# Kernel tuning notes

Hardware: AMD Instinct MI355X
Metric: run time of the kernel (lower is better)

Reference implementation:

```python
import jax, jax.numpy as jnp
import numpy as np

N = 50000
E = 1600000
HID = 128
H = 8
D = HID // H


def _layer_norm(x, g, b, eps=1e-5):
    mu = jnp.mean(x, axis=-1, keepdims=True)
    var = jnp.mean(jnp.square(x - mu), axis=-1, keepdims=True)
    return (x - mu) * jax.lax.rsqrt(var + eps) * g + b


def setup_inputs() -> dict:
    key = jax.random.key(0)
    ks = jax.random.split(key, 20)
    s = 1.0 / np.sqrt(HID)
    inp = {
        "x": jax.random.normal(ks[0], (N, HID), jnp.float32),
        "edge_index": jax.random.randint(ks[1], (2, E), 0, N, jnp.int64),
        "edge_attr": jax.random.randint(ks[2], (E,), 0, 13, jnp.int64),
        # projections (stored as [in, out] so y = x @ W + b)
        "Wq": jax.random.normal(ks[3], (HID, HID), jnp.float32) * s,
        "bq": jnp.zeros((HID,), jnp.float32),
        "Wk": jax.random.normal(ks[4], (HID, HID), jnp.float32) * s,
        "bk": jnp.zeros((HID,), jnp.float32),
        "Wv": jax.random.normal(ks[5], (HID, HID), jnp.float32) * s,
        "bv": jnp.zeros((HID,), jnp.float32),
        "Wo": jax.random.normal(ks[6], (HID, HID), jnp.float32) * s,
        "bo": jnp.zeros((HID,), jnp.float32),
        "edge_bias_table": jax.random.normal(ks[7], (13, H), jnp.float32) * 0.02,
        "W1": jax.random.normal(ks[8], (HID, 4 * HID), jnp.float32) * s,
        "b1": jnp.zeros((4 * HID,), jnp.float32),
        "W2": jax.random.normal(ks[9], (4 * HID, HID), jnp.float32) * (0.5 * s),
        "b2": jnp.zeros((HID,), jnp.float32),
        "g1": jnp.ones((HID,), jnp.float32),
        "be1": jnp.zeros((HID,), jnp.float32),
        "g2": jnp.ones((HID,), jnp.float32),
        "be2": jnp.zeros((HID,), jnp.float32),
    }
    return inp


def reference(x, edge_index, edge_attr, Wq, bq, Wk, bk, Wv, bv, Wo, bo,
              edge_bias_table, W1, b1, W2, b2, g1, be1, g2, be2):
    n = x.shape[0]
    residual = x
    h = _layer_norm(x, g1, be1)
    Q = (h @ Wq + bq).reshape(n, H, D)
    K = (h @ Wk + bk).reshape(n, H, D)
    V = (h @ Wv + bv).reshape(n, H, D)
    src, dst = edge_index[0], edge_index[1]
    # per-edge scores [E, H]
    scores = jnp.sum(Q[dst] * K[src], axis=-1) / np.sqrt(D)
    scores = scores + edge_bias_table[jnp.clip(edge_attr, 0, 12)]
    # scatter softmax over incoming edges of each dst (global max, as in source)
    scores_exp = jnp.exp(scores - jnp.max(scores))
    attn_sum = jax.ops.segment_sum(scores_exp, dst, num_segments=n)  # [N, H]
    attn_w = scores_exp / (attn_sum[dst] + 1e-8)                      # [E, H]
    messages = V[src] * attn_w[..., None]                             # [E, H, D]
    out = jax.ops.segment_sum(messages, dst, num_segments=n)          # [N, H, D]
    out = out.reshape(n, HID) @ Wo + bo
    x = residual + out  # dropout is identity in eval
    residual = x
    h2 = _layer_norm(x, g2, be2)
    ffn = jax.nn.relu(h2 @ W1 + b1) @ W2 + b2
    return residual + ffn
```

## Files before the change

### kernel.cpp

```cpp
#include <hip/hip_runtime.h>
#include <hip/hip_bf16.h>

#define N_NODES 50000
#define E_EDGES 1600000
#define HID 128
#define NH 8
#define HD 16

#define NBKT 196
#define BKT_CAP 9216
#define CHUNK_A 4096
#define EPT 16

using short8 = __attribute__((ext_vector_type(8))) short;
using f32x4  = __attribute__((ext_vector_type(4))) float;
using f32x2  = __attribute__((ext_vector_type(2))) float;
typedef _Float16 h16x2 __attribute__((ext_vector_type(2)));

#if defined(__has_builtin) && __has_builtin(__builtin_amdgcn_fdot2)
#define FDOT2(a, b, c) __builtin_amdgcn_fdot2((a), (b), (c), false)
#else
__device__ __forceinline__ float FDOT2(h16x2 a, h16x2 b, float c) {
    return fmaf((float)a[0], (float)b[0], fmaf((float)a[1], (float)b[1], c));
}
#endif

__device__ __forceinline__ float wave_reduce_sum(float v) {
    #pragma unroll
    for (int off = 32; off > 0; off >>= 1) v += __shfl_xor(v, off, 64);
    return v;
}

__device__ __forceinline__ unsigned int packbf2(float a, float b) {
    __hip_bfloat162 t;
    t.x = __float2bfloat16(a);
    t.y = __float2bfloat16(b);
    unsigned int u;
    __builtin_memcpy(&u, &t, 4);
    return u;
}

__device__ __forceinline__ unsigned char fp8e(float v) {
    return (unsigned char)(__builtin_amdgcn_cvt_pk_fp8_f32(v, v, 0u, false) & 0xFFu);
}

__device__ __forceinline__ void cvt16(uint4 u, float* f) {
    f32x2 t;
    t = __builtin_amdgcn_cvt_pk_f32_fp8(u.x, false); f[0] = t[0];  f[1] = t[1];
    t = __builtin_amdgcn_cvt_pk_f32_fp8(u.x, true);  f[2] = t[0];  f[3] = t[1];
    t = __builtin_amdgcn_cvt_pk_f32_fp8(u.y, false); f[4] = t[0];  f[5] = t[1];
    t = __builtin_amdgcn_cvt_pk_f32_fp8(u.y, true);  f[6] = t[0];  f[7] = t[1];
    t = __builtin_amdgcn_cvt_pk_f32_fp8(u.z, false); f[8] = t[0];  f[9] = t[1];
    t = __builtin_amdgcn_cvt_pk_f32_fp8(u.z, true);  f[10] = t[0]; f[11] = t[1];
    t = __builtin_amdgcn_cvt_pk_f32_fp8(u.w, false); f[12] = t[0]; f[13] = t[1];
    t = __builtin_amdgcn_cvt_pk_f32_fp8(u.w, true);  f[14] = t[0]; f[15] = t[1];
}

union U4H {
    uint4 u;
    h16x2 h[4];
};

__global__ __launch_bounds__(256) void ln_kernel(const float* __restrict__ x,
                                                 const float* __restrict__ g,
                                                 const float* __restrict__ b,
                                                 __hip_bfloat16* __restrict__ out, int n) {
    int wave = threadIdx.x >> 6;
    int lane = threadIdx.x & 63;
    int row = blockIdx.x * 4 + wave;
    if (row >= n) return;
    float2 v = ((const float2*)(x + (size_t)row * HID))[lane];
    float s = wave_reduce_sum(v.x + v.y);
    float mu = s * (1.0f / HID);
    float dx = v.x - mu, dy = v.y - mu;
    float q = wave_reduce_sum(dx * dx + dy * dy);
    float rstd = rsqrtf(q * (1.0f / HID) + 1e-5f);
    float2 gg = ((const float2*)g)[lane];
    float2 bb = ((const float2*)b)[lane];
    __hip_bfloat162 o;
    o.x = __float2bfloat16(dx * rstd * gg.x + bb.x);
    o.y = __float2bfloat16(dy * rstd * gg.y + bb.y);
    ((__hip_bfloat162*)(out + (size_t)row * HID))[lane] = o;
}

__global__ __launch_bounds__(256) void wcvt_all(const float* __restrict__ Wq,
                                                const float* __restrict__ Wk,
                                                const float* __restrict__ Wv,
                                                const float* __restrict__ Wo,
                                                const float* __restrict__ W1,
                                                const float* __restrict__ W2,
                                                const float* __restrict__ bq,
                                                const float* __restrict__ bk,
                                                const float* __restrict__ bv,
                                                __hip_bfloat16* __restrict__ Wqkvt,
                                                __hip_bfloat16* __restrict__ Wot,
                                                __hip_bfloat16* __restrict__ W1t,
                                                __hip_bfloat16* __restrict__ W2t,
                                                float* __restrict__ bqkv,
                                                int* __restrict__ bcur) {
    int t = blockIdx.x * 256 + threadIdx.x;
    if (t >= 196608) {
        int i = t - 196608;
        if (i < 384) bqkv[i] = i < 128 ? bq[i] : (i < 256 ? bk[i - 128] : bv[i - 256]);
        else if (i < 384 + NBKT) bcur[i - 384] = 0;
        return;
    }
    const float* W; __hip_bfloat16* Wt; int K, N, idx;
    if (t < 65536) {
        int which = t >> 14; idx = t & 16383; K = 128; N = 128;
        W = which == 0 ? Wq : which == 1 ? Wk : which == 2 ? Wv : Wo;
        Wt = which == 3 ? Wot : Wqkvt + which * 16384;
    } else if (t < 131072) { idx = t - 65536;  K = 128; N = 512; W = W1; Wt = W1t; }
    else                   { idx = t - 131072; K = 512; N = 128; W = W2; Wt = W2t; }
    int n = idx / K, k = idx - n * K;
    Wt[idx] = __float2bfloat16(W[(size_t)k * N + n]);
}

template <int K, int OB>
__global__ __launch_bounds__(512) void gemm_mfma(const __hip_bfloat16* __restrict__ A,
                                                 const __hip_bfloat16* __restrict__ Wt,
                                                 const float* __restrict__ bias,
                                                 const float* __restrict__ res,
                                                 float* __restrict__ C,
                                                 __hip_bfloat16* __restrict__ Cb,
                                                 _Float16* __restrict__ Chh,
                                                 unsigned char* __restrict__ C8,
                                                 const float* __restrict__ gw,
                                                 const float* __restrict__ bw,
                                                 int M, int NC, int relu) {
    __shared__ short8 smem[2048 + 2048];
    const int row0 = blockIdx.x * 128;
    const int col0 = blockIdx.y * 128;
    const int tid = threadIdx.x;
    const int w = tid >> 6, l = tid & 63;
    const int lr = l & 15, hi = l >> 4;
    f32x4 acc[8] = {};
    for (int kk = 0; kk < K / 128; ++kk) {
        #pragma unroll
        for (int it = 0; it < 4; ++it) {
            unsigned d = tid + it * 512;
            int r = d >> 4, sd = d & 15;
            int ss = sd ^ (r & 7);
            int gr = row0 + r; if (gr >= M) gr = M - 1;
            __builtin_amdgcn_global_load_lds(
                (const __attribute__((address_space(1))) void*)(A + (size_t)gr * K + kk * 128 + ss * 8),
                (__attribute__((address_space(3))) void*)(smem + (d & ~63u)),
                16, 0, 0);
        }
        #pragma unroll
        for (int it = 0; it < 4; ++it) {
            unsigned d = tid + it * 512;
            int r = d >> 4, sd = d & 15;
            int ss = sd ^ (r & 7);
            __builtin_amdgcn_global_load_lds(
                (const __attribute__((address_space(1))) void*)(Wt + (size_t)(col0 + r) * K + kk * 128 + ss * 8),
                (__attribute__((address_space(3))) void*)(smem + 2048 + (d & ~63u)),
                16, 0, 0);
        }
        __syncthreads();
        const int ar = w * 16 + lr;
        #pragma unroll
        for (int ks = 0; ks < 4; ++ks) {
            int s = ks * 4 + hi;
            short8 a = smem[ar * 16 + (s ^ (ar & 7))];
            #pragma unroll
            for (int f = 0; f < 8; ++f) {
                int br = f * 16 + lr;
                short8 b = smem[2048 + br * 16 + (s ^ (br & 7))];
                acc[f] = __builtin_amdgcn_mfma_f32_16x16x32_bf16(a, b, acc[f], 0, 0, 0);
            }
        }
        __syncthreads();
    }
    if (OB == 3) {
        float vv[8][4];
        float gc[8], bc[8];
        #pragma unroll
        for (int f = 0; f < 8; ++f) {
            int c = f * 16 + lr;
            gc[f] = gw[c]; bc[f] = bw[c];
            float bv = bias[c];
            #pragma unroll
            for (int j = 0; j < 4; ++j) {
                int r = row0 + w * 16 + hi * 4 + j;
                int rr = r < M ? r : M - 1;
                vv[f][j] = acc[f][j] + bv + res[(size_t)rr * NC + c];
            }
        }
        #pragma unroll
        for (int j = 0; j < 4; ++j) {
            int r = row0 + w * 16 + hi * 4 + j;
            float s = 0.f, qq = 0.f;
            #pragma unroll
            for (int f = 0; f < 8; ++f) { s += vv[f][j]; qq += vv[f][j] * vv[f][j]; }
            #pragma unroll
            for (int m = 1; m <= 8; m <<= 1) { s += __shfl_xor(s, m); qq += __shfl_xor(qq, m); }
            float mu = s * (1.0f / 128.0f);
            float rstd = rsqrtf(qq * (1.0f / 128.0f) - mu * mu + 1e-5f);
            if (r < M) {
                #pragma unroll
                for (int f = 0; f < 8; ++f) {
                    int c = f * 16 + lr;
                    C[(size_t)r * NC + c] = vv[f][j];
                    Cb[(size_t)r * NC + c] = __float2bfloat16((vv[f][j] - mu) * rstd * gc[f] + bc[f]);
                }
            }
        }
        return;
    }
    const float scl = (OB == 2 && blockIdx.y == 0) ? 0.25f : 1.0f;
    #pragma unroll
    for (int f = 0; f < 8; ++f) {
        int c = col0 + f * 16 + lr;
        float bv = bias[c];
        #pragma unroll
        for (int j = 0; j < 4; ++j) {
            int r = row0 + w * 16 + hi * 4 + j;
            if (r < M) {
                float v = acc[f][j] + bv;
                if (relu) v = fmaxf(v, 0.f);
                if (res) v += res[(size_t)r * NC + c];
                if (OB == 0) C[(size_t)r * NC + c] = v;
                else if (OB == 1) Cb[(size_t)r * NC + c] = __float2bfloat16(v);
                else {
                    if (blockIdx.y < 2)
                        Chh[(size_t)blockIdx.y * N_NODES * 128 + (size_t)r * 128 + (c & 127)] =
                            (_Float16)(v * scl);
                    else
                        C8[(size_t)r * 128 + (c & 127)] = fp8e(v);
                }
            }
        }
    }
}

__global__ __launch_bounds__(256) void binA_kernel(const int* __restrict__ ei,
                                                   const int* __restrict__ attr,
                                                   int* __restrict__ bcur,
                                                   unsigned int* __restrict__ temp) {
    __shared__ unsigned int sval[CHUNK_A];
    __shared__ unsigned short sbkt[CHUNK_A];
    __shared__ int hist[NBKT];
    __shared__ int lofs[NBKT];
    __shared__ int gbase[NBKT];
    __shared__ int lcur[NBKT];
    __shared__ int sc[256];
    const int tid = threadIdx.x;
    const int e0 = blockIdx.x * CHUNK_A;
    const int n = min(CHUNK_A, E_EDGES - e0);
    for (int i = tid; i < NBKT; i += 256) hist[i] = 0;
    __syncthreads();
    unsigned int v[EPT];
    short bk[EPT];
    #pragma unroll
    for (int j = 0; j < EPT; ++j) {
        int i = tid + j * 256;
        bk[j] = -1;
        v[j] = 0;
        if (i < n) {
            int e = e0 + i;
            int src = ei[e];
            int dst = ei[E_EDGES + e];
            int a = attr[e]; a = min(max(a, 0), 12);
            v[j] = (unsigned)src | ((unsigned)a << 16) | ((unsigned)(dst & 255) << 20);
            int b = dst >> 8;
            bk[j] = (short)b;
            atomicAdd(&hist[b], 1);
        }
    }
    __syncthreads();
    sc[tid] = (tid < NBKT) ? hist[tid] : 0;
    __syncthreads();
    for (int off = 1; off < 256; off <<= 1) {
        int x = (tid >= off) ? sc[tid - off] : 0;
        __syncthreads();
        sc[tid] += x;
        __syncthreads();
    }
    if (tid < NBKT) {
        int h = hist[tid];
        lofs[tid] = sc[tid] - h;
        lcur[tid] = 0;
        gbase[tid] = h ? atomicAdd(&bcur[tid], h) : 0;
    }
    __syncthreads();
    #pragma unroll
    for (int j = 0; j < EPT; ++j) {
        if (bk[j] >= 0) {
            int p = lofs[bk[j]] + atomicAdd(&lcur[bk[j]], 1);
            sval[p] = v[j];
            sbkt[p] = (unsigned short)bk[j];
        }
    }
    __syncthreads();
    for (int i = tid; i < n; i += 256) {
        int b = sbkt[i];
        temp[(size_t)b * BKT_CAP + gbase[b] + (i - lofs[b])] = sval[i];
    }
}

__global__ __launch_bounds__(1024) void binB_kernel(const int* __restrict__ bcur,
                                                    const unsigned int* __restrict__ temp,
                                                    unsigned int* __restrict__ packed,
                                                    int* __restrict__ offs) {
    __shared__ int cnts[256];
    __shared__ int hist[256];
    __shared__ int cur[256];
    const int b = blockIdx.x, tid = threadIdx.x;
    if (tid < 256) {
        cnts[tid] = (tid < NBKT) ? bcur[tid] : 0;
        hist[tid] = 0;
    }
    __syncthreads();
    for (int off = 1; off < 256; off <<= 1) {
        int x = 0;
        if (tid < 256 && tid >= off) x = cnts[tid - off];
        __syncthreads();
        if (tid < 256) cnts[tid] += x;
        __syncthreads();
    }
    const int cnt = bcur[b];
    const int start = cnts[b] - cnt;
    const size_t base = (size_t)b * BKT_CAP;
    for (int i = tid; i < cnt; i += 1024)
        atomicAdd(&hist[(temp[base + i] >> 20) & 255], 1);
    __syncthreads();
    if (tid < 256) cur[tid] = hist[tid];
    __syncthreads();
    for (int off = 1; off < 256; off <<= 1) {
        int x = 0;
        if (tid < 256 && tid >= off) x = cur[tid - off];
        __syncthreads();
        if (tid < 256) cur[tid] += x;
        __syncthreads();
    }
    const int node0 = b * 256;
    if (tid < 256) {
        int excl = cur[tid] - hist[tid];
        cur[tid] = excl;
        int node = node0 + tid;
        if (node < N_NODES) offs[node] = start + excl;
    }
    if (b == NBKT - 1 && tid == 0) offs[N_NODES] = start + cnt;
    __syncthreads();
    for (int i = tid; i < cnt; i += 1024) {
        unsigned int v = temp[base + i];
        int d = (v >> 20) & 255;
        int p = start + atomicAdd(&cur[d], 1);
        packed[p] = v & 0xFFFFFu;
    }
}

__global__ __launch_bounds__(256) void fused_attn_kernel(
    const unsigned int* __restrict__ packed,
    const int* __restrict__ offs,
    const _Float16* __restrict__ qkh,
    const unsigned char* __restrict__ v8p,
    const float* __restrict__ btab,
    __hip_bfloat16* __restrict__ out) {
    __shared__ float bLDS[104];
    const int tid = threadIdx.x;
    if (tid < 104) bLDS[tid] = btab[tid];
    __syncthreads();
    const int wave = tid >> 6, lane = tid & 63;
    const int n = blockIdx.x * 4 + wave;
    const int slot = lane >> 3, sub = lane & 7;
    const char* qh = (const char*)qkh;
    const char* kh = (const char*)(qkh + (size_t)N_NODES * 128);
    const unsigned sb = (unsigned)sub << 5;
    U4H q0, q1;
    q0.u = *(const uint4*)(qh + ((unsigned)n << 8) + sb);
    q1.u = *(const uint4*)(qh + ((unsigned)n << 8) + sb + 16u);
    const int lo = offs[n], hi = offs[n + 1];
    const int nit = (hi - lo + 7) >> 3;
    int i = lo + slot;
    float acc[16] = {};
    float wsum = 0.f;
    bool valid = i < hi;
    unsigned int pk = valid ? packed[i] : 0u;
    int i1 = i + 8;
    bool valid1 = i1 < hi;
    unsigned int pk1 = valid1 ? packed[i1] : 0u;
    unsigned src = pk & 0xFFFFu;
    U4H k0, k1;
    k0.u = *(const uint4*)(kh + (src << 8) + sb);
    k1.u = *(const uint4*)(kh + (src << 8) + sb + 16u);
    uint4 vc = *(const uint4*)(v8p + (src << 7) + (sb >> 1));
    for (int it = 0; it < nit; ++it) {
        const int i2 = i1 + 8;
        const bool valid2 = i2 < hi;
        const unsigned int pk2 = valid2 ? packed[i2] : 0u;
        const unsigned srcn = pk1 & 0xFFFFu;
        U4H kn0, kn1;
        kn0.u = *(const uint4*)(kh + (srcn << 8) + sb);
        kn1.u = *(const uint4*)(kh + (srcn << 8) + sb + 16u);
        uint4 vn = *(const uint4*)(v8p + (srcn << 7) + (sb >> 1));
        float p = 0.f;
        #pragma unroll
        for (int j = 0; j < 4; ++j) p = FDOT2(q0.h[j], k0.h[j], p);
        #pragma unroll
        for (int j = 0; j < 4; ++j) p = FDOT2(q1.h[j], k1.h[j], p);
        float s = p + bLDS[((pk >> 16) & 0xFu) * 8 + sub];
        float w = valid ? __expf(s) : 0.f;
        wsum += w;
        float v[16];
        cvt16(vc, v);
        #pragma unroll
        for (int j = 0; j < 16; ++j) acc[j] = fmaf(w, v[j], acc[j]);
        k0 = kn0; k1 = kn1; vc = vn;
        pk = pk1; valid = valid1;
        pk1 = pk2; valid1 = valid2; i1 = i2;
    }
    #pragma unroll
    for (int j = 0; j < 16; ++j) {
        acc[j] += __shfl_xor(acc[j], 8);
        acc[j] += __shfl_xor(acc[j], 16);
        acc[j] += __shfl_xor(acc[j], 32);
    }
    wsum += __shfl_xor(wsum, 8);
    wsum += __shfl_xor(wsum, 16);
    wsum += __shfl_xor(wsum, 32);
    if (slot == 0) {
        float inv = 1.0f / (wsum + 1e-8f);
        uint4 o0, o1;
        o0.x = packbf2(acc[0] * inv, acc[1] * inv);
        o0.y = packbf2(acc[2] * inv, acc[3] * inv);
        o0.z = packbf2(acc[4] * inv, acc[5] * inv);
        o0.w = packbf2(acc[6] * inv, acc[7] * inv);
        o1.x = packbf2(acc[8] * inv, acc[9] * inv);
        o1.y = packbf2(acc[10] * inv, acc[11] * inv);
        o1.z = packbf2(acc[12] * inv, acc[13] * inv);
        o1.w = packbf2(acc[14] * inv, acc[15] * inv);
        char* op = (char*)out + ((unsigned)n << 8) + ((unsigned)sub << 5);
        *(uint4*)op = o0;
        *(uint4*)(op + 16) = o1;
    }
}

extern "C" void kernel_launch(void* const* d_in, const int* in_sizes, int n_in,
                              void* d_out, int out_size, void* d_ws, size_t ws_size,
                              hipStream_t stream) {
    const float* x    = (const float*)d_in[0];
    const int*   ei   = (const int*)d_in[1];
    const int*   attr = (const int*)d_in[2];
    const float* Wq   = (const float*)d_in[3];
    const float* bq   = (const float*)d_in[4];
    const float* Wk   = (const float*)d_in[5];
    const float* bk   = (const float*)d_in[6];
    const float* Wv   = (const float*)d_in[7];
    const float* bv   = (const float*)d_in[8];
    const float* Wo   = (const float*)d_in[9];
    const float* bo   = (const float*)d_in[10];
    const float* ebt  = (const float*)d_in[11];
    const float* W1   = (const float*)d_in[12];
    const float* b1   = (const float*)d_in[13];
    const float* W2   = (const float*)d_in[14];
    const float* b2   = (const float*)d_in[15];
    const float* g1   = (const float*)d_in[16];
    const float* be1  = (const float*)d_in[17];
    const float* g2   = (const float*)d_in[18];
    const float* be2  = (const float*)d_in[19];
    float* out = (float*)d_out;

    char* ws = (char*)d_ws;
    const size_t szRowF = (size_t)N_NODES * HID * 4;
    const size_t szRowB = (size_t)N_NODES * HID * 2;
    const size_t ALIGN = 256;
    #define ALN(v) (((v) + ALIGN - 1) & ~(ALIGN - 1))
    size_t o = 0;
    __hip_bfloat16* h_buf = (__hip_bfloat16*)(ws + o); o += szRowB;
    _Float16* QKh = (_Float16*)(ws + o); o += (size_t)N_NODES * 256 * 2;
    unsigned char* V8 = (unsigned char*)(ws + o); o += (size_t)N_NODES * 128;
    unsigned int* packed = (unsigned int*)(ws + o); o += (size_t)E_EDGES * 4;
    unsigned int* temp = (unsigned int*)(ws + o); o += (size_t)NBKT * BKT_CAP * 4;
    int* bcur = (int*)(ws + o); o = ALN(o + (size_t)NBKT * 4);
    int* offs = (int*)(ws + o); o = ALN(o + (size_t)(N_NODES + 1) * 4);
    __hip_bfloat16* attn_ob = (__hip_bfloat16*)(ws + o); o += szRowB;
    float* x1 = (float*)(ws + o); o += szRowF;
    __hip_bfloat16* f1 = (__hip_bfloat16*)(ws + o); o += (size_t)N_NODES * 512 * 2;
    __hip_bfloat16* Wqkvt = (__hip_bfloat16*)(ws + o); o += 384 * 128 * 2;
    __hip_bfloat16* Wot = (__hip_bfloat16*)(ws + o); o += 128 * 128 * 2;
    __hip_bfloat16* W1t = (__hip_bfloat16*)(ws + o); o += 512 * 128 * 2;
    __hip_bfloat16* W2t = (__hip_bfloat16*)(ws + o); o += 128 * 512 * 2;
    float* bqkv = (float*)(ws + o); o += 384 * 4;
    __hip_bfloat16* h2 = h_buf;

    wcvt_all<<<771, 256, 0, stream>>>(Wq, Wk, Wv, Wo, W1, W2, bq, bk, bv,
                                      Wqkvt, Wot, W1t, W2t, bqkv, bcur);

    binA_kernel<<<(E_EDGES + CHUNK_A - 1) / CHUNK_A, 256, 0, stream>>>(ei, attr, bcur, temp);
    binB_kernel<<<NBKT, 1024, 0, stream>>>(bcur, temp, packed, offs);

    ln_kernel<<<(N_NODES + 3) / 4, 256, 0, stream>>>(x, g1, be1, h_buf, N_NODES);
    dim3 gqkv((N_NODES + 127) / 128, 3);
    gemm_mfma<128, 2><<<gqkv, 512, 0, stream>>>(h_buf, Wqkvt, bqkv, nullptr,
                                                nullptr, nullptr, QKh, V8,
                                                nullptr, nullptr, N_NODES, 384, 0);

    fused_attn_kernel<<<(N_NODES + 3) / 4, 256, 0, stream>>>(packed, offs, QKh, V8, ebt, attn_ob);

    dim3 gm((N_NODES + 127) / 128, 1);
    gemm_mfma<128, 3><<<gm, 512, 0, stream>>>(attn_ob, Wot, bo, x, x1,
                                              h2, nullptr, nullptr, g2, be2, N_NODES, 128, 0);

    dim3 gf1((N_NODES + 127) / 128, 4);
    gemm_mfma<128, 1><<<gf1, 512, 0, stream>>>(h2, W1t, b1, nullptr, nullptr,
                                               f1, nullptr, nullptr, nullptr, nullptr, N_NODES, 512, 1);
    gemm_mfma<512, 0><<<gm, 512, 0, stream>>>(f1, W2t, b2, x1, out,
                                              nullptr, nullptr, nullptr, nullptr, nullptr, N_NODES, 128, 0);
}
```

Before: 234.4 us.

## Merge binning, weight conversion and layernorm into one prep kernel; deepen attention prefetch

Three independent preprocessing kernels (edge binning, weight transpose/convert, first layernorm) are combined into a single launch that picks its role from the block index, and the bucket counters are now cleared with a memset. This removes launch gaps and lets the three independent jobs run concurrently on the GPU. The attention gather loop now prefetches K/V rows two edges ahead instead of one and accumulates with packed f32x2 FMAs, to hide more gather latency. In exchange the merged kernel reserves the binning LDS for every block, which can lower occupancy for the layernorm blocks, and the deeper prefetch uses more registers.

```diff
diff --git a/kernel.cpp b/kernel.cpp
--- a/kernel.cpp
+++ b/kernel.cpp
@@ -11,6 +11,9 @@
 #define BKT_CAP 9216
 #define CHUNK_A 4096
 #define EPT 16
+#define BINA_BLOCKS ((E_EDGES + CHUNK_A - 1) / CHUNK_A)
+#define WCVT_BLOCKS 771
+#define LN_BLOCKS 12500
 
 using short8 = __attribute__((ext_vector_type(8))) short;
 using f32x4  = __attribute__((ext_vector_type(4))) float;
@@ -44,76 +47,124 @@
     return (unsigned char)(__builtin_amdgcn_cvt_pk_fp8_f32(v, v, 0u, false) & 0xFFu);
 }
 
-__device__ __forceinline__ void cvt16(uint4 u, float* f) {
-    f32x2 t;
-    t = __builtin_amdgcn_cvt_pk_f32_fp8(u.x, false); f[0] = t[0];  f[1] = t[1];
-    t = __builtin_amdgcn_cvt_pk_f32_fp8(u.x, true);  f[2] = t[0];  f[3] = t[1];
-    t = __builtin_amdgcn_cvt_pk_f32_fp8(u.y, false); f[4] = t[0];  f[5] = t[1];
-    t = __builtin_amdgcn_cvt_pk_f32_fp8(u.y, true);  f[6] = t[0];  f[7] = t[1];
-    t = __builtin_amdgcn_cvt_pk_f32_fp8(u.z, false); f[8] = t[0];  f[9] = t[1];
-    t = __builtin_amdgcn_cvt_pk_f32_fp8(u.z, true);  f[10] = t[0]; f[11] = t[1];
-    t = __builtin_amdgcn_cvt_pk_f32_fp8(u.w, false); f[12] = t[0]; f[13] = t[1];
-    t = __builtin_amdgcn_cvt_pk_f32_fp8(u.w, true);  f[14] = t[0]; f[15] = t[1];
-}
-
 union U4H {
     uint4 u;
     h16x2 h[4];
 };
 
-__global__ __launch_bounds__(256) void ln_kernel(const float* __restrict__ x,
-                                                 const float* __restrict__ g,
-                                                 const float* __restrict__ b,
-                                                 __hip_bfloat16* __restrict__ out, int n) {
-    int wave = threadIdx.x >> 6;
-    int lane = threadIdx.x & 63;
-    int row = blockIdx.x * 4 + wave;
-    if (row >= n) return;
-    float2 v = ((const float2*)(x + (size_t)row * HID))[lane];
-    float s = wave_reduce_sum(v.x + v.y);
-    float mu = s * (1.0f / HID);
-    float dx = v.x - mu, dy = v.y - mu;
-    float q = wave_reduce_sum(dx * dx + dy * dy);
-    float rstd = rsqrtf(q * (1.0f / HID) + 1e-5f);
-    float2 gg = ((const float2*)g)[lane];
-    float2 bb = ((const float2*)b)[lane];
-    __hip_bfloat162 o;
-    o.x = __float2bfloat16(dx * rstd * gg.x + bb.x);
-    o.y = __float2bfloat16(dy * rstd * gg.y + bb.y);
-    ((__hip_bfloat162*)(out + (size_t)row * HID))[lane] = o;
-}
-
-__global__ __launch_bounds__(256) void wcvt_all(const float* __restrict__ Wq,
-                                                const float* __restrict__ Wk,
-                                                const float* __restrict__ Wv,
-                                                const float* __restrict__ Wo,
-                                                const float* __restrict__ W1,
-                                                const float* __restrict__ W2,
-                                                const float* __restrict__ bq,
-                                                const float* __restrict__ bk,
-                                                const float* __restrict__ bv,
-                                                __hip_bfloat16* __restrict__ Wqkvt,
-                                                __hip_bfloat16* __restrict__ Wot,
-                                                __hip_bfloat16* __restrict__ W1t,
-                                                __hip_bfloat16* __restrict__ W2t,
-                                                float* __restrict__ bqkv,
-                                                int* __restrict__ bcur) {
-    int t = blockIdx.x * 256 + threadIdx.x;
-    if (t >= 196608) {
-        int i = t - 196608;
-        if (i < 384) bqkv[i] = i < 128 ? bq[i] : (i < 256 ? bk[i - 128] : bv[i - 256]);
-        else if (i < 384 + NBKT) bcur[i - 384] = 0;
-        return;
-    }
-    const float* W; __hip_bfloat16* Wt; int K, N, idx;
-    if (t < 65536) {
-        int which = t >> 14; idx = t & 16383; K = 128; N = 128;
-        W = which == 0 ? Wq : which == 1 ? Wk : which == 2 ? Wv : Wo;
-        Wt = which == 3 ? Wot : Wqkvt + which * 16384;
-    } else if (t < 131072) { idx = t - 65536;  K = 128; N = 512; W = W1; Wt = W1t; }
-    else                   { idx = t - 131072; K = 512; N = 128; W = W2; Wt = W2t; }
-    int n = idx / K, k = idx - n * K;
-    Wt[idx] = __float2bfloat16(W[(size_t)k * N + n]);
+struct KV {
+    U4H k0, k1;
+    uint4 v;
+};
+
+__global__ __launch_bounds__(256) void prep_kernel(
+    const int* __restrict__ ei, const int* __restrict__ attr,
+    int* __restrict__ bcur, unsigned int* __restrict__ temp,
+    const float* __restrict__ Wq, const float* __restrict__ Wk,
+    const float* __restrict__ Wv, const float* __restrict__ Wo,
+    const float* __restrict__ W1, const float* __restrict__ W2,
+    const float* __restrict__ bq, const float* __restrict__ bk,
+    const float* __restrict__ bv,
+    __hip_bfloat16* __restrict__ Wqkvt, __hip_bfloat16* __restrict__ Wot,
+    __hip_bfloat16* __restrict__ W1t, __hip_bfloat16* __restrict__ W2t,
+    float* __restrict__ bqkv,
+    const float* __restrict__ x, const float* __restrict__ g1,
+    const float* __restrict__ be1, __hip_bfloat16* __restrict__ h_out) {
+    __shared__ unsigned int sval[CHUNK_A];
+    __shared__ unsigned short sbkt[CHUNK_A];
+    __shared__ int hist[NBKT];
+    __shared__ int lofs[NBKT];
+    __shared__ int gbase[NBKT];
+    __shared__ int lcur[NBKT];
+    __shared__ int sc[256];
+    const int b = blockIdx.x;
+    const int tid = threadIdx.x;
+    if (b < BINA_BLOCKS) {
+        const int e0 = b * CHUNK_A;
+        const int n = min(CHUNK_A, E_EDGES - e0);
+        for (int i = tid; i < NBKT; i += 256) hist[i] = 0;
+        __syncthreads();
+        unsigned int v[EPT];
+        short bk_[EPT];
+        #pragma unroll
+        for (int j = 0; j < EPT; ++j) {
+            int i = tid + j * 256;
+            bk_[j] = -1;
+            v[j] = 0;
+            if (i < n) {
+                int e = e0 + i;
+                int src = ei[e];
+                int dst = ei[E_EDGES + e];
+                int a = attr[e]; a = min(max(a, 0), 12);
+                v[j] = (unsigned)src | ((unsigned)a << 16) | ((unsigned)(dst & 255) << 20);
+                int bb = dst >> 8;
+                bk_[j] = (short)bb;
+                atomicAdd(&hist[bb], 1);
+            }
+        }
+        __syncthreads();
+        sc[tid] = (tid < NBKT) ? hist[tid] : 0;
+        __syncthreads();
+        for (int off = 1; off < 256; off <<= 1) {
+            int xx = (tid >= off) ? sc[tid - off] : 0;
+            __syncthreads();
+            sc[tid] += xx;
+            __syncthreads();
+        }
+        if (tid < NBKT) {
+            int h = hist[tid];
+            lofs[tid] = sc[tid] - h;
+            lcur[tid] = 0;
+            gbase[tid] = h ? atomicAdd(&bcur[tid], h) : 0;
+        }
+        __syncthreads();
+        #pragma unroll
+        for (int j = 0; j < EPT; ++j) {
+            if (bk_[j] >= 0) {
+                int p = lofs[bk_[j]] + atomicAdd(&lcur[bk_[j]], 1);
+                sval[p] = v[j];
+                sbkt[p] = (unsigned short)bk_[j];
+            }
+        }
+        __syncthreads();
+        for (int i = tid; i < n; i += 256) {
+            int bb = sbkt[i];
+            temp[(size_t)bb * BKT_CAP + gbase[bb] + (i - lofs[bb])] = sval[i];
+        }
+    } else if (b < BINA_BLOCKS + WCVT_BLOCKS) {
+        int t = (b - BINA_BLOCKS) * 256 + tid;
+        if (t >= 196608) {
+            int i = t - 196608;
+            if (i < 384) bqkv[i] = i < 128 ? bq[i] : (i < 256 ? bk[i - 128] : bv[i - 256]);
+            return;
+        }
+        const float* W; __hip_bfloat16* Wt; int K, N, idx;
+        if (t < 65536) {
+            int which = t >> 14; idx = t & 16383; K = 128; N = 128;
+            W = which == 0 ? Wq : which == 1 ? Wk : which == 2 ? Wv : Wo;
+            Wt = which == 3 ? Wot : Wqkvt + which * 16384;
+        } else if (t < 131072) { idx = t - 65536;  K = 128; N = 512; W = W1; Wt = W1t; }
+        else                   { idx = t - 131072; K = 512; N = 128; W = W2; Wt = W2t; }
+        int n = idx / K, k = idx - n * K;
+        Wt[idx] = __float2bfloat16(W[(size_t)k * N + n]);
+    } else {
+        int wave = tid >> 6;
+        int lane = tid & 63;
+        int row = (b - BINA_BLOCKS - WCVT_BLOCKS) * 4 + wave;
+        if (row >= N_NODES) return;
+        float2 v = ((const float2*)(x + (size_t)row * HID))[lane];
+        float s = wave_reduce_sum(v.x + v.y);
+        float mu = s * (1.0f / HID);
+        float dx = v.x - mu, dy = v.y - mu;
+        float q = wave_reduce_sum(dx * dx + dy * dy);
+        float rstd = rsqrtf(q * (1.0f / HID) + 1e-5f);
+        float2 gg = ((const float2*)g1)[lane];
+        float2 bb = ((const float2*)be1)[lane];
+        __hip_bfloat162 o;
+        o.x = __float2bfloat16(dx * rstd * gg.x + bb.x);
+        o.y = __float2bfloat16(dy * rstd * gg.y + bb.y);
+        ((__hip_bfloat162*)(h_out + (size_t)row * HID))[lane] = o;
+    }
 }
 
 template <int K, int OB>
@@ -231,71 +282,6 @@
                 }
             }
         }
-    }
-}
-
-__global__ __launch_bounds__(256) void binA_kernel(const int* __restrict__ ei,
-                                                   const int* __restrict__ attr,
-                                                   int* __restrict__ bcur,
-                                                   unsigned int* __restrict__ temp) {
-    __shared__ unsigned int sval[CHUNK_A];
-    __shared__ unsigned short sbkt[CHUNK_A];
-    __shared__ int hist[NBKT];
-    __shared__ int lofs[NBKT];
-    __shared__ int gbase[NBKT];
-    __shared__ int lcur[NBKT];
-    __shared__ int sc[256];
-    const int tid = threadIdx.x;
-    const int e0 = blockIdx.x * CHUNK_A;
-    const int n = min(CHUNK_A, E_EDGES - e0);
-    for (int i = tid; i < NBKT; i += 256) hist[i] = 0;
-    __syncthreads();
-    unsigned int v[EPT];
-    short bk[EPT];
-    #pragma unroll
-    for (int j = 0; j < EPT; ++j) {
-        int i = tid + j * 256;
-        bk[j] = -1;
-        v[j] = 0;
-        if (i < n) {
-            int e = e0 + i;
-            int src = ei[e];
-            int dst = ei[E_EDGES + e];
-            int a = attr[e]; a = min(max(a, 0), 12);
-            v[j] = (unsigned)src | ((unsigned)a << 16) | ((unsigned)(dst & 255) << 20);
-            int b = dst >> 8;
-            bk[j] = (short)b;
-            atomicAdd(&hist[b], 1);
-        }
-    }
-    __syncthreads();
-    sc[tid] = (tid < NBKT) ? hist[tid] : 0;
-    __syncthreads();
-    for (int off = 1; off < 256; off <<= 1) {
-        int x = (tid >= off) ? sc[tid - off] : 0;
-        __syncthreads();
-        sc[tid] += x;
-        __syncthreads();
-    }
-    if (tid < NBKT) {
-        int h = hist[tid];
-        lofs[tid] = sc[tid] - h;
-        lcur[tid] = 0;
-        gbase[tid] = h ? atomicAdd(&bcur[tid], h) : 0;
-    }
-    __syncthreads();
-    #pragma unroll
-    for (int j = 0; j < EPT; ++j) {
-        if (bk[j] >= 0) {
-            int p = lofs[bk[j]] + atomicAdd(&lcur[bk[j]], 1);
-            sval[p] = v[j];
-            sbkt[p] = (unsigned short)bk[j];
-        }
-    }
-    __syncthreads();
-    for (int i = tid; i < n; i += 256) {
-        int b = sbkt[i];
-        temp[(size_t)b * BKT_CAP + gbase[b] + (i - lofs[b])] = sval[i];
     }
 }
 
@@ -373,49 +359,66 @@
     q1.u = *(const uint4*)(qh + ((unsigned)n << 8) + sb + 16u);
     const int lo = offs[n], hi = offs[n + 1];
     const int nit = (hi - lo + 7) >> 3;
-    int i = lo + slot;
-    float acc[16] = {};
+    f32x2 acc2[8] = {};
     float wsum = 0.f;
-    bool valid = i < hi;
-    unsigned int pk = valid ? packed[i] : 0u;
-    int i1 = i + 8;
-    bool valid1 = i1 < hi;
-    unsigned int pk1 = valid1 ? packed[i1] : 0u;
-    unsigned src = pk & 0xFFFFu;
-    U4H k0, k1;
-    k0.u = *(const uint4*)(kh + (src << 8) + sb);
-    k1.u = *(const uint4*)(kh + (src << 8) + sb + 16u);
-    uint4 vc = *(const uint4*)(v8p + (src << 7) + (sb >> 1));
+    int i0 = lo + slot;
+    bool vd0 = i0 < hi;           unsigned pk0 = vd0 ? packed[i0] : 0u;
+    bool vd1 = i0 + 8 < hi;       unsigned pk1 = vd1 ? packed[i0 + 8] : 0u;
+    bool vd2 = i0 + 16 < hi;      unsigned pk2 = vd2 ? packed[i0 + 16] : 0u;
+    int inext = i0 + 24;
+    KV kv0, kv1;
+    {
+        unsigned r0 = (pk0 & 0xFFFFu);
+        kv0.k0.u = *(const uint4*)(kh + (r0 << 8) + sb);
+        kv0.k1.u = *(const uint4*)(kh + (r0 << 8) + sb + 16u);
+        kv0.v = *(const uint4*)(v8p + (r0 << 7) + (sb >> 1));
+        unsigned r1 = (pk1 & 0xFFFFu);
+        kv1.k0.u = *(const uint4*)(kh + (r1 << 8) + sb);
+        kv1.k1.u = *(const uint4*)(kh + (r1 << 8) + sb + 16u);
+        kv1.v = *(const uint4*)(v8p + (r1 << 7) + (sb >> 1));
+    }
     for (int it = 0; it < nit; ++it) {
-        const int i2 = i1 + 8;
-        const bool valid2 = i2 < hi;
-        const unsigned int pk2 = valid2 ? packed[i2] : 0u;
-        const unsigned srcn = pk1 & 0xFFFFu;
-        U4H kn0, kn1;
-        kn0.u = *(const uint4*)(kh + (srcn << 8) + sb);
-        kn1.u = *(const uint4*)(kh + (srcn << 8) + sb + 16u);
-        uint4 vn = *(const uint4*)(v8p + (srcn << 7) + (sb >> 1));
+        const bool vd3 = inext < hi;
+        const unsigned pk3 = vd3 ? packed[inext] : 0u;
+        KV kv2;
+        {
+            unsigned r2 = (pk2 & 0xFFFFu);
+            kv2.k0.u = *(const uint4*)(kh + (r2 << 8) + sb);
+            kv2.k1.u = *(const uint4*)(kh + (r2 << 8) + sb + 16u);
+            kv2.v = *(const uint4*)(v8p + (r2 << 7) + (sb >> 1));
+        }
         float p = 0.f;
         #pragma unroll
-        for (int j = 0; j < 4; ++j) p = FDOT2(q0.h[j], k0.h[j], p);
-        #pragma unroll
-        for (int j = 0; j < 4; ++j) p = FDOT2(q1.h[j], k1.h[j], p);
-        float s = p + bLDS[((pk >> 16) & 0xFu) * 8 + sub];
-        float w = valid ? __expf(s) : 0.f;
+        for (int j = 0; j < 4; ++j) p = FDOT2(q0.h[j], kv0.k0.h[j], p);
+        #pragma unroll
+        for (int j = 0; j < 4; ++j) p = FDOT2(q1.h[j], kv0.k1.h[j], p);
+        float s = p + bLDS[((pk0 >> 16) & 0xFu) * 8 + sub];
+        float w = vd0 ? __expf(s) : 0.f;
         wsum += w;
-        float v[16];
-        cvt16(vc, v);
-        #pragma unroll
-        for (int j = 0; j < 16; ++j) acc[j] = fmaf(w, v[j], acc[j]);
-        k0 = kn0; k1 = kn1; vc = vn;
-        pk = pk1; valid = valid1;
-        pk1 = pk2; valid1 = valid2; i1 = i2;
-    }
+        f32x2 w2; w2[0] = w; w2[1] = w;
+        f32x2 t;
+        t = __builtin_amdgcn_cvt_pk_f32_fp8(kv0.v.x, false); acc2[0] = t * w2 + acc2[0];
+        t = __builtin_amdgcn_cvt_pk_f32_fp8(kv0.v.x, true);  acc2[1] = t * w2 + acc2[1];
+        t = __builtin_amdgcn_cvt_pk_f32_fp8(kv0.v.y, false); acc2[2] = t * w2 + acc2[2];
+        t = __builtin_amdgcn_cvt_pk_f32_fp8(kv0.v.y, true);  acc2[3] = t * w2 + acc2[3];
+        t = __builtin_amdgcn_cvt_pk_f32_fp8(kv0.v.z, false); acc2[4] = t * w2 + acc2[4];
+        t = __builtin_amdgcn_cvt_pk_f32_fp8(kv0.v.z, true);  acc2[5] = t * w2 + acc2[5];
+        t = __builtin_amdgcn_cvt_pk_f32_fp8(kv0.v.w, false); acc2[6] = t * w2 + acc2[6];
+        t = __builtin_amdgcn_cvt_pk_f32_fp8(kv0.v.w, true);  acc2[7] = t * w2 + acc2[7];
+        pk0 = pk1; vd0 = vd1;
+        pk1 = pk2; vd1 = vd2;
+        pk2 = pk3; vd2 = vd3;
+        kv0 = kv1; kv1 = kv2;
+        inext += 8;
+    }
+    float accf[16];
+    #pragma unroll
+    for (int j = 0; j < 8; ++j) { accf[2 * j] = acc2[j][0]; accf[2 * j + 1] = acc2[j][1]; }
     #pragma unroll
     for (int j = 0; j < 16; ++j) {
-        acc[j] += __shfl_xor(acc[j], 8);
-        acc[j] += __shfl_xor(acc[j], 16);
-        acc[j] += __shfl_xor(acc[j], 32);
+        accf[j] += __shfl_xor(accf[j], 8);
+        accf[j] += __shfl_xor(accf[j], 16);
+        accf[j] += __shfl_xor(accf[j], 32);
     }
     wsum += __shfl_xor(wsum, 8);
     wsum += __shfl_xor(wsum, 16);
@@ -423,14 +426,14 @@
     if (slot == 0) {
         float inv = 1.0f / (wsum + 1e-8f);
         uint4 o0, o1;
-        o0.x = packbf2(acc[0] * inv, acc[1] * inv);
-        o0.y = packbf2(acc[2] * inv, acc[3] * inv);
-        o0.z = packbf2(acc[4] * inv, acc[5] * inv);
-        o0.w = packbf2(acc[6] * inv, acc[7] * inv);
-        o1.x = packbf2(acc[8] * inv, acc[9] * inv);
-        o1.y = packbf2(acc[10] * inv, acc[11] * inv);
-        o1.z = packbf2(acc[12] * inv, acc[13] * inv);
-        o1.w = packbf2(acc[14] * inv, acc[15] * inv);
+        o0.x = packbf2(accf[0] * inv, accf[1] * inv);
+        o0.y = packbf2(accf[2] * inv, accf[3] * inv);
+        o0.z = packbf2(accf[4] * inv, accf[5] * inv);
+        o0.w = packbf2(accf[6] * inv, accf[7] * inv);
+        o1.x = packbf2(accf[8] * inv, accf[9] * inv);
+        o1.y = packbf2(accf[10] * inv, accf[11] * inv);
+        o1.z = packbf2(accf[12] * inv, accf[13] * inv);
+        o1.w = packbf2(accf[14] * inv, accf[15] * inv);
         char* op = (char*)out + ((unsigned)n << 8) + ((unsigned)sub << 5);
         *(uint4*)op = o0;
         *(uint4*)(op + 16) = o1;
@@ -485,13 +488,16 @@
     float* bqkv = (float*)(ws + o); o += 384 * 4;
     __hip_bfloat16* h2 = h_buf;
 
-    wcvt_all<<<771, 256, 0, stream>>>(Wq, Wk, Wv, Wo, W1, W2, bq, bk, bv,
-                                      Wqkvt, Wot, W1t, W2t, bqkv, bcur);
-
-    binA_kernel<<<(E_EDGES + CHUNK_A - 1) / CHUNK_A, 256, 0, stream>>>(ei, attr, bcur, temp);
+    hipMemsetAsync(bcur, 0, (size_t)NBKT * 4, stream);
+
+    prep_kernel<<<BINA_BLOCKS + WCVT_BLOCKS + LN_BLOCKS, 256, 0, stream>>>(
+        ei, attr, bcur, temp,
+        Wq, Wk, Wv, Wo, W1, W2, bq, bk, bv,
+        Wqkvt, Wot, W1t, W2t, bqkv,
+        x, g1, be1, h_buf);
+
     binB_kernel<<<NBKT, 1024, 0, stream>>>(bcur, temp, packed, offs);
 
-    ln_kernel<<<(N_NODES + 3) / 4, 256, 0, stream>>>(x, g1, be1, h_buf, N_NODES);
     dim3 gqkv((N_NODES + 127) / 128, 3);
     gemm_mfma<128, 2><<<gqkv, 512, 0, stream>>>(h_buf, Wqkvt, bqkv, nullptr,
                                                 nullptr, nullptr, QKh, V8,
```

New measurement: 228.4 us. 1.03x faster.
